# Kernel optimization log

Measured on AMD Instinct MI355X. Metric: run time of the kernel, lower is better.

Reference implementation:

```python
import jax, jax.numpy as jnp
import numpy as np

B, T, C, H = 4, 2048, 1024, 16
DH = C // H  # 64


def setup_inputs() -> dict:
    key = jax.random.key(0)
    ks = jax.random.split(key, 9)
    s = 1.0 / np.sqrt(C)
    return {
        "x": jax.random.normal(ks[0], (B, T, C), dtype=jnp.float32),
        "Wq": jax.random.normal(ks[1], (C, C), dtype=jnp.float32) * s,
        "bq": jax.random.normal(ks[2], (C,), dtype=jnp.float32) * 0.01,
        "Wk": jax.random.normal(ks[3], (C, C), dtype=jnp.float32) * s,
        "bk": jax.random.normal(ks[4], (C,), dtype=jnp.float32) * 0.01,
        "Wv": jax.random.normal(ks[5], (C, C), dtype=jnp.float32) * s,
        "bv": jax.random.normal(ks[6], (C,), dtype=jnp.float32) * 0.01,
        "Wo": jax.random.normal(ks[7], (C, C), dtype=jnp.float32) * s,
        "bo": jax.random.normal(ks[8], (C,), dtype=jnp.float32) * 0.01,
    }


def reference(x, Wq, bq, Wk, bk, Wv, bv, Wo, bo):
    b, t, c = x.shape
    # q,k,v: [B, H, T, DH]
    def heads(W, bias):
        return (x @ W.T + bias).reshape(b, t, H, DH).transpose(0, 2, 1, 3)
    q = heads(Wq, bq)
    k = heads(Wk, bk)
    v = heads(Wv, bv)
    scale = 1.0 / np.sqrt(DH)
    att = jnp.einsum('bhqd,bhkd->bhqk', q, k) * scale  # [B,H,T,T]
    # causal mask (is_causal=True)
    causal = jnp.tril(jnp.ones((t, t), dtype=bool))
    att = jnp.where(causal[None, None], att, -jnp.inf)
    att = jax.nn.softmax(att, axis=-1)
    y = jnp.einsum('bhqk,bhkd->bhqd', att, v)  # [B,H,T,DH]
    y = y.transpose(0, 2, 1, 3).reshape(b, t, c)
    return y @ Wo.T + bo
```

## Files before the change

### kernel.cpp

```cpp
#include <hip/hip_runtime.h>


typedef _Float16 fp16x8 __attribute__((ext_vector_type(8)));
typedef _Float16 fp16x4 __attribute__((ext_vector_type(4)));
typedef _Float16 fp16x2 __attribute__((ext_vector_type(2)));
typedef float f32x4 __attribute__((ext_vector_type(4)));

#define LOG2E 1.44269504088896f
#define M_FIX 10.0f

__device__ __forceinline__ void async_ld16(const _Float16* g, _Float16* l) {
  __builtin_amdgcn_global_load_lds(
      (const __attribute__((address_space(1))) void*)g,
      (__attribute__((address_space(3))) void*)l, 16, 0, 0);
}

__global__ __launch_bounds__(256) void cast_all(
    const float* __restrict__ x, const float* __restrict__ wq, const float* __restrict__ wk,
    const float* __restrict__ wv, const float* __restrict__ wo,
    _Float16* __restrict__ xh, _Float16* __restrict__ wcat, _Float16* __restrict__ woh) {
  const int bid = blockIdx.x;
  const float* s;
  _Float16* d;
  int off;
  if (bid < 4096) {
    s = x; d = xh; off = bid * 2048;
  } else {
    const int t = bid - 4096;
    const int wi = t >> 9;
    off = (t & 511) * 2048;
    s = (wi == 0) ? wq : (wi == 1) ? wk : (wi == 2) ? wv : wo;
    d = (wi < 3) ? (wcat + wi * 1048576) : woh;
  }
  const int i = off + threadIdx.x * 8;
  float4 a = *(const float4*)(s + i);
  float4 b = *(const float4*)(s + i + 4);
  fp16x8 h;
  h[0] = (_Float16)a.x; h[1] = (_Float16)a.y; h[2] = (_Float16)a.z; h[3] = (_Float16)a.w;
  h[4] = (_Float16)b.x; h[5] = (_Float16)b.y; h[6] = (_Float16)b.z; h[7] = (_Float16)b.w;
  *(fp16x8*)(d + i) = h;
}

__global__ __launch_bounds__(256) void gemm_qkv(
    const _Float16* __restrict__ A, const _Float16* __restrict__ W,
    const float* __restrict__ bq, const float* __restrict__ bk, const float* __restrict__ bv,
    _Float16* __restrict__ qo, _Float16* __restrict__ ko, _Float16* __restrict__ vo) {
  __shared__ __align__(16) _Float16 smem[16384];
  _Float16* As = smem;
  _Float16* Bs = smem + 4096;
  const int tid = threadIdx.x;
  const int m0 = blockIdx.x * 128;
  const int n0 = blockIdx.y * 128;
  const int w = tid >> 6, lane = tid & 63;
  const int lr = lane & 15, quad = lane >> 4;
  const int wm = (w & 1) * 64, wn = (w >> 1) * 64;

  f32x4 acc[4][4];
#pragma unroll
  for (int i = 0; i < 4; ++i)
#pragma unroll
    for (int j = 0; j < 4; ++j) acc[i][j] = (f32x4){0.f, 0.f, 0.f, 0.f};

  const int sr1 = tid >> 2, sc = (tid & 3) * 8, sr2 = sr1 + 64;
  const _Float16* Ag1 = A + (size_t)(m0 + sr1) * 1024 + sc;
  const _Float16* Ag2 = A + (size_t)(m0 + sr2) * 1024 + sc;
  const _Float16* Bg1 = W + (size_t)(n0 + sr1) * 1024 + sc;
  const _Float16* Bg2 = W + (size_t)(n0 + sr2) * 1024 + sc;
  _Float16* Ad1 = &As[sr1 * 32 + sc];
  _Float16* Ad2 = &As[sr2 * 32 + sc];
  _Float16* Bd1 = &Bs[sr1 * 32 + sc];
  _Float16* Bd2 = &Bs[sr2 * 32 + sc];

  for (int kt = 0; kt < 32; ++kt) {
    const int kk = kt * 32;
    __syncthreads();
    async_ld16(Ag1 + kk, Ad1);
    async_ld16(Ag2 + kk, Ad2);
    async_ld16(Bg1 + kk, Bd1);
    async_ld16(Bg2 + kk, Bd2);
    __syncthreads();
    fp16x8 af[4], bf[4];
#pragma unroll
    for (int i = 0; i < 4; ++i) {
      af[i] = *(const fp16x8*)&As[(wm + i * 16 + lr) * 32 + quad * 8];
      bf[i] = *(const fp16x8*)&Bs[(wn + i * 16 + lr) * 32 + quad * 8];
    }
#pragma unroll
    for (int i = 0; i < 4; ++i)
#pragma unroll
      for (int j = 0; j < 4; ++j)
        acc[i][j] = __builtin_amdgcn_mfma_f32_16x16x32_f16(af[i], bf[j], acc[i][j], 0, 0, 0);
  }

  const int wsel = n0 >> 10;
  const float* bias = (wsel == 0) ? bq : (wsel == 1) ? bk : bv;
  _Float16* dst = (wsel == 0) ? qo : (wsel == 1) ? ko : vo;
  float bv4[4];
#pragma unroll
  for (int j = 0; j < 4; ++j) bv4[j] = bias[(n0 + wn + j * 16 + lr) & 1023];

  __syncthreads();
  _Float16* Tr = smem + w * 4096;
#pragma unroll
  for (int j = 0; j < 4; ++j) {
    const int C = j * 16 + lr, ch = C >> 3, cin = C & 7;
#pragma unroll
    for (int i = 0; i < 4; ++i)
#pragma unroll
      for (int r = 0; r < 4; ++r) {
        const int R = i * 16 + quad * 4 + r;
        Tr[R * 64 + ((ch ^ (R & 7)) << 3) + cin] = (_Float16)(acc[i][j][r] + bv4[j]);
      }
  }
  const int r8 = lane >> 3, c8 = lane & 7;
  const int h = ((n0 + wn) & 1023) >> 6;
#pragma unroll
  for (int ch = 0; ch < 8; ++ch) {
    const int Rl = ch * 8 + r8;
    fp16x8 vv = *(const fp16x8*)&Tr[Rl * 64 + ((c8 ^ r8) << 3)];
    const int m = m0 + wm + Rl;
    const int b = m >> 11, t = m & 2047;
    *(fp16x8*)&dst[((size_t)(b * 16 + h) * 2048 + t) * 64 + c8 * 8] = vv;
  }
}

__global__ __launch_bounds__(256) void gemm_out(
    const _Float16* __restrict__ A, const _Float16* __restrict__ W,
    const float* __restrict__ bo, float* __restrict__ out) {
  __shared__ __align__(16) _Float16 smem[16384];
  _Float16* As = smem;
  _Float16* Bs = smem + 4096;
  const int tid = threadIdx.x;
  const int m0 = blockIdx.x * 128;
  const int n0 = blockIdx.y * 128;
  const int w = tid >> 6, lane = tid & 63;
  const int lr = lane & 15, quad = lane >> 4;
  const int wm = (w & 1) * 64, wn = (w >> 1) * 64;

  f32x4 acc[4][4];
#pragma unroll
  for (int i = 0; i < 4; ++i)
#pragma unroll
    for (int j = 0; j < 4; ++j) acc[i][j] = (f32x4){0.f, 0.f, 0.f, 0.f};

  const int sr1 = tid >> 2, sc = (tid & 3) * 8, sr2 = sr1 + 64;
  const _Float16* Ag1 = A + (size_t)(m0 + sr1) * 1024 + sc;
  const _Float16* Ag2 = A + (size_t)(m0 + sr2) * 1024 + sc;
  const _Float16* Bg1 = W + (size_t)(n0 + sr1) * 1024 + sc;
  const _Float16* Bg2 = W + (size_t)(n0 + sr2) * 1024 + sc;
  _Float16* Ad1 = &As[sr1 * 32 + sc];
  _Float16* Ad2 = &As[sr2 * 32 + sc];
  _Float16* Bd1 = &Bs[sr1 * 32 + sc];
  _Float16* Bd2 = &Bs[sr2 * 32 + sc];

  for (int kt = 0; kt < 32; ++kt) {
    const int kk = kt * 32;
    __syncthreads();
    async_ld16(Ag1 + kk, Ad1);
    async_ld16(Ag2 + kk, Ad2);
    async_ld16(Bg1 + kk, Bd1);
    async_ld16(Bg2 + kk, Bd2);
    __syncthreads();
    fp16x8 af[4], bf[4];
#pragma unroll
    for (int i = 0; i < 4; ++i) {
      af[i] = *(const fp16x8*)&As[(wm + i * 16 + lr) * 32 + quad * 8];
      bf[i] = *(const fp16x8*)&Bs[(wn + i * 16 + lr) * 32 + quad * 8];
    }
#pragma unroll
    for (int i = 0; i < 4; ++i)
#pragma unroll
      for (int j = 0; j < 4; ++j)
        acc[i][j] = __builtin_amdgcn_mfma_f32_16x16x32_f16(af[i], bf[j], acc[i][j], 0, 0, 0);
  }

  float bv4[4];
#pragma unroll
  for (int j = 0; j < 4; ++j) bv4[j] = bo[n0 + wn + j * 16 + lr];

  __syncthreads();
  float* Trf = (float*)smem + w * 2048;
  const int r16 = lane >> 4, c16 = lane & 15;
#pragma unroll
  for (int t2 = 0; t2 < 2; ++t2) {
#pragma unroll
    for (int i2 = 0; i2 < 2; ++i2) {
      const int i = t2 * 2 + i2;
#pragma unroll
      for (int j = 0; j < 4; ++j) {
        const int C = j * 16 + lr, ch = C >> 2, cin = C & 3;
#pragma unroll
        for (int r = 0; r < 4; ++r) {
          const int R = i2 * 16 + quad * 4 + r;
          Trf[R * 64 + ((ch ^ (R & 15)) << 2) + cin] = acc[i][j][r] + bv4[j];
        }
      }
    }
#pragma unroll
    for (int ch4 = 0; ch4 < 8; ++ch4) {
      const int Rl = ch4 * 4 + r16;
      float4 vv = *(const float4*)&Trf[Rl * 64 + ((c16 ^ (Rl & 15)) << 2)];
      *(float4*)&out[(size_t)(m0 + wm + t2 * 32 + Rl) * 1024 + n0 + wn + c16 * 4] = vv;
    }
  }
}

__global__ __launch_bounds__(256) void attn(
    const _Float16* __restrict__ q, const _Float16* __restrict__ k,
    const _Float16* __restrict__ v, _Float16* __restrict__ y) {
  __shared__ __align__(16) _Float16 Ks[64 * 64];
  __shared__ __align__(16) _Float16 Vt[64 * 64];
  const int tid = threadIdx.x;
  const int w = tid >> 6, lane = tid & 63;
  const int lr = lane & 15, quad = lane >> 4;
  const int lr7 = lr & 7;
  const int bx = blockIdx.x;
  const int bh = blockIdx.y;
  const int b = bh >> 4, h = bh & 15;
  const size_t base = (size_t)bh * 2048 * 64;

  const int mlo = bx * 64 + w * 16;
  const int mhi = (31 - bx) * 64 + w * 16;

  const int kr = tid >> 2, kcb = (tid & 3) * 16, kch = (tid & 3) * 2;
  const int vkp = (tid & 31) * 2, vdb8 = (tid >> 5) * 8;
  const int vch = (tid & 31) >> 2, vin = vkp & 7;

  const _Float16 qs = (_Float16)(0.125f * LOG2E);
  fp16x8 qlo[2], qhi[2];
#pragma unroll
  for (int c = 0; c < 2; ++c) {
    fp16x8 t0 = *(const fp16x8*)(q + base + (size_t)(mlo + lr) * 64 + c * 32 + quad * 8);
    fp16x8 t1 = *(const fp16x8*)(q + base + (size_t)(mhi + lr) * 64 + c * 32 + quad * 8);
#pragma unroll
    for (int i = 0; i < 8; ++i) { t0[i] = t0[i] * qs; t1[i] = t1[i] * qs; }
    qlo[c] = t0; qhi[c] = t1;
  }

  int voff[4];
#pragma unroll
  for (int kct = 0; kct < 4; ++kct)
    voff[kct] = (((kct * 2 + (quad >> 1)) ^ lr7) << 3) + (quad & 1) * 4;

  f32x4 olo[4], ohi[4];
#pragma unroll
  for (int dt = 0; dt < 4; ++dt) {
    olo[dt] = (f32x4){0.f, 0.f, 0.f, 0.f};
    ohi[dt] = (f32x4){0.f, 0.f, 0.f, 0.f};
  }
  float lplo = 0.f, lphi = 0.f;

  const int ntiles = 32 - bx;
  fp16x8 ka, kb, va, vb;
  {
    const _Float16* kg = k + base + (size_t)kr * 64 + kcb;
    const _Float16* vg = v + base + (size_t)vkp * 64 + vdb8;
    ka = *(const fp16x8*)kg; kb = *(const fp16x8*)(kg + 8);
    va = *(const fp16x8*)vg; vb = *(const fp16x8*)(vg + 64);
  }

  const f32x4 cinit = (f32x4){-M_FIX, -M_FIX, -M_FIX, -M_FIX};

  for (int kt = 0; kt < ntiles; ++kt) {
    __syncthreads();
    *(fp16x8*)&Ks[kr * 64 + ((kch ^ (kr & 7)) << 3)] = ka;
    *(fp16x8*)&Ks[kr * 64 + (((kch + 1) ^ (kr & 7)) << 3)] = kb;
#pragma unroll
    for (int i = 0; i < 8; ++i) {
      fp16x2 p; p[0] = va[i]; p[1] = vb[i];
      *(fp16x2*)&Vt[(vdb8 + i) * 64 + ((vch ^ i) << 3) + vin] = p;
    }
    __syncthreads();
    if (kt + 1 < ntiles) {
      const _Float16* kg = k + base + (size_t)((kt + 1) * 64 + kr) * 64 + kcb;
      const _Float16* vg = v + base + (size_t)((kt + 1) * 64 + vkp) * 64 + vdb8;
      ka = *(const fp16x8*)kg; kb = *(const fp16x8*)(kg + 8);
      va = *(const fp16x8*)vg; vb = *(const fp16x8*)(vg + 64);
    }

    const bool lo_on = (kt <= bx);
    f32x4 shi[4], slo[4];
#pragma unroll
    for (int kct = 0; kct < 4; ++kct) {
      fp16x8 kf0 = *(const fp16x8*)&Ks[(kct * 16 + lr) * 64 + ((quad ^ lr7) << 3)];
      fp16x8 kf1 = *(const fp16x8*)&Ks[(kct * 16 + lr) * 64 + (((4 + quad) ^ lr7) << 3)];
      shi[kct] = __builtin_amdgcn_mfma_f32_16x16x32_f16(kf0, qhi[0], cinit, 0, 0, 0);
      shi[kct] = __builtin_amdgcn_mfma_f32_16x16x32_f16(kf1, qhi[1], shi[kct], 0, 0, 0);
      if (lo_on) {
        slo[kct] = __builtin_amdgcn_mfma_f32_16x16x32_f16(kf0, qlo[0], cinit, 0, 0, 0);
        slo[kct] = __builtin_amdgcn_mfma_f32_16x16x32_f16(kf1, qlo[1], slo[kct], 0, 0, 0);
      }
    }

    {
      const bool dmask = (kt == ntiles - 1);
      const int qrow = mhi + lr;
#pragma unroll
      for (int kct = 0; kct < 4; ++kct) {
        const int kc0 = kt * 64 + kct * 16 + quad * 4;
        fp16x4 pf;
#pragma unroll
        for (int r = 0; r < 4; ++r) {
          float p = __builtin_amdgcn_exp2f(shi[kct][r]);
          if (dmask && (kc0 + r) > qrow) p = 0.f;
          lphi += p;
          pf[r] = (_Float16)p;
        }
#pragma unroll
        for (int dt = 0; dt < 4; ++dt) {
          fp16x4 af = *(const fp16x4*)&Vt[(dt * 16 + lr) * 64 + voff[kct]];
          ohi[dt] = __builtin_amdgcn_mfma_f32_16x16x16f16(af, pf, ohi[dt], 0, 0, 0);
        }
      }
    }
    if (lo_on) {
      const bool dmask = (kt == bx);
      const int qrow = mlo + lr;
#pragma unroll
      for (int kct = 0; kct < 4; ++kct) {
        const int kc0 = kt * 64 + kct * 16 + quad * 4;
        fp16x4 pf;
#pragma unroll
        for (int r = 0; r < 4; ++r) {
          float p = __builtin_amdgcn_exp2f(slo[kct][r]);
          if (dmask && (kc0 + r) > qrow) p = 0.f;
          lplo += p;
          pf[r] = (_Float16)p;
        }
#pragma unroll
        for (int dt = 0; dt < 4; ++dt) {
          fp16x4 af = *(const fp16x4*)&Vt[(dt * 16 + lr) * 64 + voff[kct]];
          olo[dt] = __builtin_amdgcn_mfma_f32_16x16x16f16(af, pf, olo[dt], 0, 0, 0);
        }
      }
    }
  }

  lplo += __shfl_xor(lplo, 16); lplo += __shfl_xor(lplo, 32);
  lphi += __shfl_xor(lphi, 16); lphi += __shfl_xor(lphi, 32);
  const float ilo = 1.f / lplo, ihi = 1.f / lphi;

  _Float16* yplo = y + ((size_t)(b * 2048 + mlo + lr)) * 1024 + h * 64;
  _Float16* yphi = y + ((size_t)(b * 2048 + mhi + lr)) * 1024 + h * 64;
#pragma unroll
  for (int dt = 0; dt < 4; ++dt) {
    fp16x4 slo4, shi4;
#pragma unroll
    for (int r = 0; r < 4; ++r) {
      slo4[r] = (_Float16)(olo[dt][r] * ilo);
      shi4[r] = (_Float16)(ohi[dt][r] * ihi);
    }
    *(fp16x4*)&yplo[dt * 16 + quad * 4] = slo4;
    *(fp16x4*)&yphi[dt * 16 + quad * 4] = shi4;
  }
}

extern "C" void kernel_launch(void* const* d_in, const int* in_sizes, int n_in,
                              void* d_out, int out_size, void* d_ws, size_t ws_size,
                              hipStream_t stream) {
  const float* x  = (const float*)d_in[0];
  const float* Wq = (const float*)d_in[1];
  const float* bq = (const float*)d_in[2];
  const float* Wk = (const float*)d_in[3];
  const float* bk = (const float*)d_in[4];
  const float* Wv = (const float*)d_in[5];
  const float* bv = (const float*)d_in[6];
  const float* Wo = (const float*)d_in[7];
  const float* bo = (const float*)d_in[8];

  _Float16* ws   = (_Float16*)d_ws;
  _Float16* xh   = ws;
  _Float16* Wcat = xh + 8388608;
  _Float16* Woh  = Wcat + 3145728;
  _Float16* qh   = Woh + 1048576;
  _Float16* kh   = qh + 8388608;
  _Float16* vh   = kh + 8388608;
  _Float16* yh   = xh;

  cast_all<<<6144, 256, 0, stream>>>(x, Wq, Wk, Wv, Wo, xh, Wcat, Woh);
  gemm_qkv<<<dim3(64, 24), 256, 0, stream>>>(xh, Wcat, bq, bk, bv, qh, kh, vh);
  attn<<<dim3(16, 64), 256, 0, stream>>>(qh, kh, vh, yh);
  gemm_out<<<dim3(64, 8), 256, 0, stream>>>(yh, Woh, bo, (float*)d_out);
}
```

Measured before the change: 276.1 us.

## Double-buffer K/V via async global-to-LDS loads and transposed LDS reads

The attention kernel now loads K and V tiles straight into double-buffered LDS with global_load_lds, replacing register staging and the manual transposed scatter of V. One barrier per tile is used instead of two. The PV matrix multiply reads V through ds_read_b64_tr_b16, which transposes on the fly. MFMA sections are wrapped in s_setprio and sched barriers to improve overlap. This doubles LDS use, which may reduce occupancy, and relies on the V layout in LDS matching the hard-coded transposed-read offsets.

```diff
diff --git a/kernel.cpp b/kernel.cpp
--- a/kernel.cpp
+++ b/kernel.cpp
@@ -205,11 +205,49 @@
   }
 }
 
+typedef __attribute__((address_space(3))) _Float16 lds_f16;
+
+#define PVSTEP(KCT, OFF0, OFF1, OFF2, OFF3)                                        \
+  {                                                                                \
+    fp16x4 g0, g1, g2, g3;                                                         \
+    asm volatile("ds_read_b64_tr_b16 %0, %1 offset:" OFF0                          \
+                 : "=v"(g0) : "v"(vtp) : "memory");                                \
+    asm volatile("ds_read_b64_tr_b16 %0, %1 offset:" OFF1                          \
+                 : "=v"(g1) : "v"(vtp) : "memory");                                \
+    asm volatile("ds_read_b64_tr_b16 %0, %1 offset:" OFF2                          \
+                 : "=v"(g2) : "v"(vtp) : "memory");                                \
+    asm volatile("ds_read_b64_tr_b16 %0, %1 offset:" OFF3                          \
+                 : "=v"(g3) : "v"(vtp) : "memory");                                \
+    float p0 = __builtin_amdgcn_exp2f(s[KCT][0]);                                  \
+    float p1 = __builtin_amdgcn_exp2f(s[KCT][1]);                                  \
+    float p2 = __builtin_amdgcn_exp2f(s[KCT][2]);                                  \
+    float p3 = __builtin_amdgcn_exp2f(s[KCT][3]);                                  \
+    if (dmask) {                                                                   \
+      const int kc0 = kb + KCT * 16 + quad * 4;                                    \
+      if (kc0 + 0 > qrow) p0 = 0.f;                                                \
+      if (kc0 + 1 > qrow) p1 = 0.f;                                                \
+      if (kc0 + 2 > qrow) p2 = 0.f;                                                \
+      if (kc0 + 3 > qrow) p3 = 0.f;                                                \
+    }                                                                              \
+    lp += (p0 + p1) + (p2 + p3);                                                   \
+    fp16x4 pf;                                                                     \
+    pf[0] = (_Float16)p0; pf[1] = (_Float16)p1;                                    \
+    pf[2] = (_Float16)p2; pf[3] = (_Float16)p3;                                    \
+    asm volatile("s_waitcnt lgkmcnt(0)" ::: "memory");                             \
+    __builtin_amdgcn_sched_barrier(0);                                             \
+    __builtin_amdgcn_s_setprio(1);                                                 \
+    o[0] = __builtin_amdgcn_mfma_f32_16x16x16f16(g0, pf, o[0], 0, 0, 0);           \
+    o[1] = __builtin_amdgcn_mfma_f32_16x16x16f16(g1, pf, o[1], 0, 0, 0);           \
+    o[2] = __builtin_amdgcn_mfma_f32_16x16x16f16(g2, pf, o[2], 0, 0, 0);           \
+    o[3] = __builtin_amdgcn_mfma_f32_16x16x16f16(g3, pf, o[3], 0, 0, 0);           \
+    __builtin_amdgcn_s_setprio(0);                                                 \
+  }
+
 __global__ __launch_bounds__(256) void attn(
     const _Float16* __restrict__ q, const _Float16* __restrict__ k,
     const _Float16* __restrict__ v, _Float16* __restrict__ y) {
-  __shared__ __align__(16) _Float16 Ks[64 * 64];
-  __shared__ __align__(16) _Float16 Vt[64 * 64];
+  __shared__ __align__(16) _Float16 smem[16384];
+  _Float16* sm = smem;
   const int tid = threadIdx.x;
   const int w = tid >> 6, lane = tid & 63;
   const int lr = lane & 15, quad = lane >> 4;
@@ -222,9 +260,20 @@
   const int mlo = bx * 64 + w * 16;
   const int mhi = (31 - bx) * 64 + w * 16;
 
-  const int kr = tid >> 2, kcb = (tid & 3) * 16, kch = (tid & 3) * 2;
-  const int vkp = (tid & 31) * 2, vdb8 = (tid >> 5) * 8;
-  const int vch = (tid & 31) >> 2, vin = vkp & 7;
+  const int kr_a = 2 * w * 8 + (lane >> 3);
+  const int ksw = (((lane & 7) ^ (lane >> 3)) << 3);
+  const _Float16* kp0 = k + base + (size_t)kr_a * 64 + ksw;
+  const _Float16* kp1 = kp0 + 8 * 64;
+  const _Float16* vp0 = v + base + (size_t)(lane >> 1) * 64 + w * 16 + (lane & 1) * 8;
+  const _Float16* vp1 = vp0 + (size_t)32 * 64;
+  const int kdA = 2 * w * 512 + lane * 8, kdB = kdA + 512;
+  const int vdA = w * 1024 + lane * 8, vdB = vdA + 512;
+
+  async_ld16(kp0, sm + kdA);
+  async_ld16(kp1, sm + kdB);
+  async_ld16(vp0, sm + 8192 + vdA);
+  async_ld16(vp1, sm + 8192 + vdB);
+  kp0 += 4096; kp1 += 4096; vp0 += 4096; vp1 += 4096;
 
   const _Float16 qs = (_Float16)(0.125f * LOG2E);
   fp16x8 qlo[2], qhi[2];
@@ -237,10 +286,8 @@
     qlo[c] = t0; qhi[c] = t1;
   }
 
-  int voff[4];
-#pragma unroll
-  for (int kct = 0; kct < 4; ++kct)
-    voff[kct] = (((kct * 2 + (quad >> 1)) ^ lr7) << 3) + (quad & 1) * 4;
+  const lds_f16* vbase =
+      (const lds_f16*)(smem + 8192 + quad * 64 + (lr >> 2) * 16 + (lr & 3) * 4);
 
   f32x4 olo[4], ohi[4];
 #pragma unroll
@@ -250,90 +297,46 @@
   }
   float lplo = 0.f, lphi = 0.f;
 
+  const f32x4 cinit = (f32x4){-M_FIX, -M_FIX, -M_FIX, -M_FIX};
   const int ntiles = 32 - bx;
-  fp16x8 ka, kb, va, vb;
-  {
-    const _Float16* kg = k + base + (size_t)kr * 64 + kcb;
-    const _Float16* vg = v + base + (size_t)vkp * 64 + vdb8;
-    ka = *(const fp16x8*)kg; kb = *(const fp16x8*)(kg + 8);
-    va = *(const fp16x8*)vg; vb = *(const fp16x8*)(vg + 64);
-  }
-
-  const f32x4 cinit = (f32x4){-M_FIX, -M_FIX, -M_FIX, -M_FIX};
+  int bsel = 0;
 
   for (int kt = 0; kt < ntiles; ++kt) {
-    __syncthreads();
-    *(fp16x8*)&Ks[kr * 64 + ((kch ^ (kr & 7)) << 3)] = ka;
-    *(fp16x8*)&Ks[kr * 64 + (((kch + 1) ^ (kr & 7)) << 3)] = kb;
-#pragma unroll
-    for (int i = 0; i < 8; ++i) {
-      fp16x2 p; p[0] = va[i]; p[1] = vb[i];
-      *(fp16x2*)&Vt[(vdb8 + i) * 64 + ((vch ^ i) << 3) + vin] = p;
-    }
+    asm volatile("s_waitcnt vmcnt(0) lgkmcnt(0)" ::: "memory");
     __syncthreads();
     if (kt + 1 < ntiles) {
-      const _Float16* kg = k + base + (size_t)((kt + 1) * 64 + kr) * 64 + kcb;
-      const _Float16* vg = v + base + (size_t)((kt + 1) * 64 + vkp) * 64 + vdb8;
-      ka = *(const fp16x8*)kg; kb = *(const fp16x8*)(kg + 8);
-      va = *(const fp16x8*)vg; vb = *(const fp16x8*)(vg + 64);
-    }
-
-    const bool lo_on = (kt <= bx);
-    f32x4 shi[4], slo[4];
-#pragma unroll
-    for (int kct = 0; kct < 4; ++kct) {
-      fp16x8 kf0 = *(const fp16x8*)&Ks[(kct * 16 + lr) * 64 + ((quad ^ lr7) << 3)];
-      fp16x8 kf1 = *(const fp16x8*)&Ks[(kct * 16 + lr) * 64 + (((4 + quad) ^ lr7) << 3)];
-      shi[kct] = __builtin_amdgcn_mfma_f32_16x16x32_f16(kf0, qhi[0], cinit, 0, 0, 0);
-      shi[kct] = __builtin_amdgcn_mfma_f32_16x16x32_f16(kf1, qhi[1], shi[kct], 0, 0, 0);
-      if (lo_on) {
-        slo[kct] = __builtin_amdgcn_mfma_f32_16x16x32_f16(kf0, qlo[0], cinit, 0, 0, 0);
-        slo[kct] = __builtin_amdgcn_mfma_f32_16x16x32_f16(kf1, qlo[1], slo[kct], 0, 0, 0);
+      const int st = bsel ^ 4096;
+      async_ld16(kp0, sm + st + kdA);
+      async_ld16(kp1, sm + st + kdB);
+      async_ld16(vp0, sm + 8192 + st + vdA);
+      async_ld16(vp1, sm + 8192 + st + vdB);
+      kp0 += 4096; kp1 += 4096; vp0 += 4096; vp1 += 4096;
+    }
+    const _Float16* KsC = sm + bsel;
+    const lds_f16* vtp = vbase + bsel;
+    const int kb = kt * 64;
+
+    auto process = [&](const fp16x8 (&qf)[2], f32x4 (&o)[4], float& lp,
+                       const int qrow, const bool dmask) {
+      f32x4 s[4];
+#pragma unroll
+      for (int kct = 0; kct < 4; ++kct) {
+        fp16x8 kf0 = *(const fp16x8*)&KsC[(kct * 16 + lr) * 64 + ((quad ^ lr7) << 3)];
+        fp16x8 kf1 = *(const fp16x8*)&KsC[(kct * 16 + lr) * 64 + (((4 + quad) ^ lr7) << 3)];
+        __builtin_amdgcn_s_setprio(1);
+        s[kct] = __builtin_amdgcn_mfma_f32_16x16x32_f16(kf0, qf[0], cinit, 0, 0, 0);
+        s[kct] = __builtin_amdgcn_mfma_f32_16x16x32_f16(kf1, qf[1], s[kct], 0, 0, 0);
+        __builtin_amdgcn_s_setprio(0);
       }
-    }
-
-    {
-      const bool dmask = (kt == ntiles - 1);
-      const int qrow = mhi + lr;
-#pragma unroll
-      for (int kct = 0; kct < 4; ++kct) {
-        const int kc0 = kt * 64 + kct * 16 + quad * 4;
-        fp16x4 pf;
-#pragma unroll
-        for (int r = 0; r < 4; ++r) {
-          float p = __builtin_amdgcn_exp2f(shi[kct][r]);
-          if (dmask && (kc0 + r) > qrow) p = 0.f;
-          lphi += p;
-          pf[r] = (_Float16)p;
-        }
-#pragma unroll
-        for (int dt = 0; dt < 4; ++dt) {
-          fp16x4 af = *(const fp16x4*)&Vt[(dt * 16 + lr) * 64 + voff[kct]];
-          ohi[dt] = __builtin_amdgcn_mfma_f32_16x16x16f16(af, pf, ohi[dt], 0, 0, 0);
-        }
-      }
-    }
-    if (lo_on) {
-      const bool dmask = (kt == bx);
-      const int qrow = mlo + lr;
-#pragma unroll
-      for (int kct = 0; kct < 4; ++kct) {
-        const int kc0 = kt * 64 + kct * 16 + quad * 4;
-        fp16x4 pf;
-#pragma unroll
-        for (int r = 0; r < 4; ++r) {
-          float p = __builtin_amdgcn_exp2f(slo[kct][r]);
-          if (dmask && (kc0 + r) > qrow) p = 0.f;
-          lplo += p;
-          pf[r] = (_Float16)p;
-        }
-#pragma unroll
-        for (int dt = 0; dt < 4; ++dt) {
-          fp16x4 af = *(const fp16x4*)&Vt[(dt * 16 + lr) * 64 + voff[kct]];
-          olo[dt] = __builtin_amdgcn_mfma_f32_16x16x16f16(af, pf, olo[dt], 0, 0, 0);
-        }
-      }
-    }
+      PVSTEP(0, "0", "2048", "4096", "6144")
+      PVSTEP(1, "512", "2560", "4608", "6656")
+      PVSTEP(2, "1024", "3072", "5120", "7168")
+      PVSTEP(3, "1536", "3584", "5632", "7680")
+    };
+
+    process(qhi, ohi, lphi, mhi + lr, kt == ntiles - 1);
+    if (kt <= bx) process(qlo, olo, lplo, mlo + lr, kt == bx);
+    bsel ^= 4096;
   }
 
   lplo += __shfl_xor(lplo, 16); lplo += __shfl_xor(lplo, 32);
```

Measured after the change: 261.0 us. -5.5%, faster.
